# Performance work log

Hardware: AMD Instinct MI355X
Metric: run time of the kernel (lower is better)

## Reference

```python
import jax, jax.numpy as jnp
import numpy as np

B, S, D, H = 4, 1024, 1024, 16
DK = D // H
MASK_WEIGHT_0 = 1.0   # weight for key-type 0 (from (weight, mask_mat) tuple)
MASK_WEIGHT_1 = 0.5   # weight for key-type 1
NEG_INF = -1.0e9


def setup_inputs() -> dict:
    key = jax.random.key(0)
    ks = jax.random.split(key, 10)
    wscale = 0.02
    return {
        "query": jax.random.normal(ks[0], (B, S, D), jnp.float32),
        "key_x": jax.random.normal(ks[1], (B, S, D), jnp.float32),
        "value": jax.random.normal(ks[2], (B, S, D), jnp.float32),
        "mask0": jax.random.randint(ks[3], (B, S, S), 0, 2, jnp.int32),
        "mask1": jax.random.randint(ks[4], (B, S, S), 0, 2, jnp.int32),
        "Wq":  wscale * jax.random.normal(ks[5], (D, D), jnp.float32),
        "Wk0": wscale * jax.random.normal(ks[6], (D, D), jnp.float32),
        "Wk1": wscale * jax.random.normal(ks[7], (D, D), jnp.float32),
        "Wv":  wscale * jax.random.normal(ks[8], (D, D), jnp.float32),
        "Wo":  wscale * jax.random.normal(ks[9], (D, D), jnp.float32),
    }


def _heads(x, W):
    # torch nn.Linear: x @ W.T ; then view(B,S,H,DK).transpose(1,2)
    return (x @ W.T).reshape(B, S, H, DK).transpose(0, 2, 1, 3)  # [B,H,S,DK]


def reference(query, key_x, value, mask0, mask1, Wq, Wk0, Wk1, Wv, Wo):
    q = _heads(query, Wq)          # [B,H,S,DK]
    k0 = _heads(key_x, Wk0)
    k1 = _heads(key_x, Wk1)
    v = _heads(value, Wv)
    scale = 1.0 / jnp.sqrt(jnp.float32(DK))

    def masked_score(k, mask, weight):
        s = jnp.einsum('bhqd,bhkd->bhqk', q, k) * scale       # [B,H,S,S]
        keep = (mask != 0)[:, None, :, :]                     # broadcast over heads
        # (score * weight*keep).masked_fill(mask==0, -1e9)
        return jnp.where(keep, s * weight, NEG_INF)

    scores = masked_score(k0, mask0, MASK_WEIGHT_0) + masked_score(k1, mask1, MASK_WEIGHT_1)
    p_attn = jax.nn.sigmoid(scores)                           # activation='sigmoid'
    x = jnp.einsum('bhqk,bhkd->bhqd', p_attn, v)              # [B,H,S,DK]
    x = x.transpose(0, 2, 1, 3).reshape(B, S, D)
    return x @ Wo.T                                            # output_linear (dropout p=0)
```

## Files before the change

### kernel.cpp

```cpp
#include <hip/hip_runtime.h>

#define B_  4
#define S_  1024
#define D_  1024
#define H_  16
#define DK_ 64

typedef __attribute__((ext_vector_type(8)))  short bf16x8;
typedef __attribute__((ext_vector_type(4)))  short bf16x4;
typedef __attribute__((ext_vector_type(4)))  float f32x4;
typedef __attribute__((ext_vector_type(16))) float f32x16;

static __device__ __forceinline__ unsigned short f2bf(float f) {
  union { float f; unsigned u; } v; v.f = f;
  unsigned r = v.u + 0x7FFFu + ((v.u >> 16) & 1u);
  return (unsigned short)(r >> 16);
}

static __device__ __forceinline__ unsigned cvtpk(float lo, float hi) {
  unsigned r;
  asm("v_cvt_pk_bf16_f32 %0, %1, %2" : "=v"(r) : "v"(lo), "v"(hi));
  return r;
}
static __device__ __forceinline__ void plswap(unsigned &a, unsigned &b) {
  asm volatile("v_permlane32_swap_b32 %0, %1" : "+v"(a), "+v"(b));
}

typedef __attribute__((address_space(1))) const void gc_t;
typedef __attribute__((address_space(3))) void lds_t;
static __device__ __forceinline__ void gload_lds16(const void* g, void* l) {
  __builtin_amdgcn_global_load_lds((gc_t*)g, (lds_t*)l, 16, 0, 0);
}

#define TM_ (1u << 22)
#define WM_ (1u << 20)

#define CEXP_ (-0.18033688011112042f)

__global__ __launch_bounds__(256)
void prep(const float* __restrict__ q, const float* __restrict__ k,
          const float* __restrict__ v,
          const float* __restrict__ w0, const float* __restrict__ w1,
          const float* __restrict__ w2, const float* __restrict__ w3,
          const float* __restrict__ w4, unsigned short* __restrict__ out,
          const int* __restrict__ m0, const int* __restrict__ m1,
          unsigned long long* __restrict__ pk)
{
  if (blockIdx.x < 8192) {
    const size_t u = ((size_t)blockIdx.x * 256 + threadIdx.x) * 8;
    unsigned short t[8];
    unsigned short* dst;
    size_t off;
    if (u < (size_t)3 * TM_) {
      int seg = (int)(u >> 22); off = u & (TM_ - 1);
      const float* src = seg == 0 ? q : (seg == 1 ? k : v);
      dst = out + (size_t)seg * TM_ + off;
      float4 f0 = *(const float4*)(src + off);
      float4 f1 = *(const float4*)(src + off + 4);
      t[0]=f2bf(f0.x); t[1]=f2bf(f0.y); t[2]=f2bf(f0.z); t[3]=f2bf(f0.w);
      t[4]=f2bf(f1.x); t[5]=f2bf(f1.y); t[6]=f2bf(f1.z); t[7]=f2bf(f1.w);
    } else {
      size_t uu = u - (size_t)3 * TM_;
      int seg = (int)(uu >> 20); off = uu & (WM_ - 1);
      dst = out + (size_t)3 * TM_ + (size_t)seg * WM_ + off;
      if (seg == 1) {
        float4 a0 = *(const float4*)(w1 + off);
        float4 a1 = *(const float4*)(w1 + off + 4);
        float4 b0 = *(const float4*)(w2 + off);
        float4 b1 = *(const float4*)(w2 + off + 4);
        t[0]=f2bf(a0.x+0.5f*b0.x); t[1]=f2bf(a0.y+0.5f*b0.y);
        t[2]=f2bf(a0.z+0.5f*b0.z); t[3]=f2bf(a0.w+0.5f*b0.w);
        t[4]=f2bf(a1.x+0.5f*b1.x); t[5]=f2bf(a1.y+0.5f*b1.y);
        t[6]=f2bf(a1.z+0.5f*b1.z); t[7]=f2bf(a1.w+0.5f*b1.w);
      } else {
        const float* src = seg == 0 ? w0 : (seg == 2 ? w3 : w4);
        float4 f0 = *(const float4*)(src + off);
        float4 f1 = *(const float4*)(src + off + 4);
        t[0]=f2bf(f0.x); t[1]=f2bf(f0.y); t[2]=f2bf(f0.z); t[3]=f2bf(f0.w);
        t[4]=f2bf(f1.x); t[5]=f2bf(f1.y); t[6]=f2bf(f1.z); t[7]=f2bf(f1.w);
      }
    }
    *(bf16x8*)dst = *(bf16x8*)t;
  } else {
    const int bidm = blockIdx.x - 8192;
    const int wid  = bidm * 4 + (threadIdx.x >> 6);
    const int lane = threadIdx.x & 63;
    const int word = wid & 15, row = wid >> 4;
    const size_t g = (size_t)row * S_ + word * 64 + lane;
    const bool bit = (m0[g] != 0) & (m1[g] != 0);
    const unsigned long long m = __ballot(bit);
    if (lane == 0) pk[wid] = m;
  }
}

__global__ __launch_bounds__(256, 4)
void proj_gemm(const unsigned short* __restrict__ qbf,
               const unsigned short* __restrict__ kbf,
               const unsigned short* __restrict__ vbf,
               const unsigned short* __restrict__ wbf,
               unsigned short* __restrict__ Qb, unsigned short* __restrict__ Kh,
               unsigned short* __restrict__ Vth)
{
  __shared__ unsigned short As[128][64];
  __shared__ unsigned short Ws[128][64];

  const int tid = threadIdx.x, bid = blockIdx.x;
  const int xcd = bid & 7, c = bid >> 3;
  const int L = xcd * 96 + c;
  const int which = L >> 8;
  const int rem = L & 255;
  const int nt = rem >> 5, mt = rem & 31;
  const int m0 = mt * 128, n0 = nt * 128;
  const int w = tid >> 6, l = tid & 63;
  const int lr = l & 15, lg = l >> 4;
  const int wr = w >> 1, wc = w & 1;

  const unsigned short* A = (which == 0) ? qbf : (which == 1) ? kbf : vbf;
  const unsigned short* W = wbf + (size_t)which * WM_;

  const f32x4 fzero = {0.f, 0.f, 0.f, 0.f};
  f32x4 acc[4][4];
#pragma unroll
  for (int m = 0; m < 4; m++)
#pragma unroll
    for (int n = 0; n < 4; n++) acc[m][n] = fzero;

  const int srow8 = l >> 3;
  const int sg    = ((l & 7) ^ srow8) * 8;
  const int rc0 = ((lg)     ^ (lr & 7)) * 8;
  const int rc1 = ((4 + lg) ^ (lr & 7)) * 8;

  const unsigned short* aBase = A + (size_t)(m0 + w*32 + srow8) * 1024 + sg;
  const unsigned short* wBase = W + (size_t)(n0 + w*32 + srow8) * 1024 + sg;

  for (int kk = 0; kk < 1024; kk += 64) {
#pragma unroll
    for (int cc = 0; cc < 4; ++cc)
      gload_lds16(aBase + (size_t)cc * 8 * 1024 + kk, &As[w*32 + cc*8][0]);
#pragma unroll
    for (int cc = 0; cc < 4; ++cc)
      gload_lds16(wBase + (size_t)cc * 8 * 1024 + kk, &Ws[w*32 + cc*8][0]);
    __syncthreads();

#pragma unroll
    for (int ks = 0; ks < 2; ++ks) {
      const int rc = ks ? rc1 : rc0;
      bf16x8 af[4], bfr[4];
#pragma unroll
      for (int m = 0; m < 4; m++) af[m]  = *(const bf16x8*)&As[wr*64 + m*16 + lr][rc];
#pragma unroll
      for (int n = 0; n < 4; n++) bfr[n] = *(const bf16x8*)&Ws[wc*64 + n*16 + lr][rc];
#pragma unroll
      for (int m = 0; m < 4; m++)
#pragma unroll
        for (int n = 0; n < 4; n++)
          acc[m][n] = __builtin_amdgcn_mfma_f32_16x16x32_bf16(af[m], bfr[n], acc[m][n], 0, 0, 0);
    }
    __syncthreads();
  }

  if (which == 2) {
#pragma unroll
    for (int m = 0; m < 4; m++) {
      const int row = m0 + wr*64 + m*16 + lg*4;
      const int b = row >> 10, s = row & 1023;
#pragma unroll
      for (int n = 0; n < 4; n++) {
        const int col = n0 + wc*64 + n*16 + lr;
        const int h = col >> 6, dk = col & 63;
        unsigned short tv[4] = {f2bf(acc[m][n][0]), f2bf(acc[m][n][1]),
                                f2bf(acc[m][n][2]), f2bf(acc[m][n][3])};
        const size_t a = ((size_t)((b*H_ + h)*DK_ + dk)) * S_
                       + (size_t)(s & ~63) + ((((s >> 3) & 7) ^ (dk & 7)) << 3) + (s & 7);
        *(bf16x4*)(Vth + a) = *(bf16x4*)tv;
      }
    }
  } else if (which == 0) {
#pragma unroll
    for (int m = 0; m < 4; m++) {
      const int row = m0 + wr*64 + m*16 + lg*4;
#pragma unroll
      for (int n = 0; n < 4; n++) {
        const int col = n0 + wc*64 + n*16 + lr;
#pragma unroll
        for (int r = 0; r < 4; r++)
          Qb[(size_t)(row + r) * 1024 + col] = f2bf(acc[m][n][r]);
      }
    }
  } else {
#pragma unroll
    for (int m = 0; m < 4; m++) {
      const int row = m0 + wr*64 + m*16 + lg*4;
#pragma unroll
      for (int n = 0; n < 4; n++) {
        const int col = n0 + wc*64 + n*16 + lr;
        const int h = col >> 6, dk = col & 63;
#pragma unroll
        for (int r = 0; r < 4; r++) {
          const int rr = row + r;
          const int b = rr >> 10, s = rr & 1023;
          const size_t a = ((size_t)((b*H_ + h)*S_ + s)) * 64
                         + (((dk >> 3) ^ (s & 7)) << 3) + (dk & 7);
          Kh[a] = f2bf(acc[m][n][r]);
        }
      }
    }
  }
}

__global__ __launch_bounds__(256, 4)
void out_gemm(const unsigned short* __restrict__ A,
              const unsigned short* __restrict__ W, float* __restrict__ C)
{
  __shared__ unsigned short As[128][64];
  __shared__ unsigned short Ws2[64][64];

  const int tid = threadIdx.x, bid = blockIdx.x;
  const int xcd = bid & 7, idx = bid >> 3;
  const int mt = (xcd << 2) | (idx & 3);
  const int nt = idx >> 2;
  const int m0 = mt * 128, n0 = nt * 64;
  const int w = tid >> 6, l = tid & 63;
  const int lr = l & 15, lg = l >> 4;
  const int wr = w >> 1, wc = w & 1;

  const f32x4 fzero = {0.f, 0.f, 0.f, 0.f};
  f32x4 acc[4][2];
#pragma unroll
  for (int m = 0; m < 4; m++)
#pragma unroll
    for (int n = 0; n < 2; n++) acc[m][n] = fzero;

  const int srow8 = l >> 3;
  const int sg    = ((l & 7) ^ srow8) * 8;
  const int rc0 = ((lg)     ^ (lr & 7)) * 8;
  const int rc1 = ((4 + lg) ^ (lr & 7)) * 8;

  const unsigned short* aBase = A + (size_t)(m0 + w*32 + srow8) * 1024 + sg;
  const unsigned short* wBase = W + (size_t)(n0 + w*16 + srow8) * 1024 + sg;

  for (int kk = 0; kk < 1024; kk += 64) {
#pragma unroll
    for (int cc = 0; cc < 4; ++cc)
      gload_lds16(aBase + (size_t)cc * 8 * 1024 + kk, &As[w*32 + cc*8][0]);
#pragma unroll
    for (int cc = 0; cc < 2; ++cc)
      gload_lds16(wBase + (size_t)cc * 8 * 1024 + kk, &Ws2[w*16 + cc*8][0]);
    __syncthreads();

#pragma unroll
    for (int ks = 0; ks < 2; ++ks) {
      const int rc = ks ? rc1 : rc0;
      bf16x8 af[4], bfr[2];
#pragma unroll
      for (int m = 0; m < 4; m++) af[m]  = *(const bf16x8*)&As[wr*64 + m*16 + lr][rc];
#pragma unroll
      for (int n = 0; n < 2; n++) bfr[n] = *(const bf16x8*)&Ws2[wc*32 + n*16 + lr][rc];
#pragma unroll
      for (int m = 0; m < 4; m++)
#pragma unroll
        for (int n = 0; n < 2; n++)
          acc[m][n] = __builtin_amdgcn_mfma_f32_16x16x32_bf16(af[m], bfr[n], acc[m][n], 0, 0, 0);
    }
    __syncthreads();
  }

#pragma unroll
  for (int m = 0; m < 4; m++) {
    const int row = m0 + wr*64 + m*16 + lg*4;
#pragma unroll
    for (int n = 0; n < 2; n++) {
      const int col = n0 + wc*32 + n*16 + lr;
#pragma unroll
      for (int r = 0; r < 4; r++)
        C[(size_t)(row + r) * 1024 + col] = acc[m][n][r];
    }
  }
}

__global__ __launch_bounds__(256)
void attn_kernel(const unsigned short* __restrict__ Q,
                 const unsigned short* __restrict__ Kh,
                 const unsigned short* __restrict__ Vth,
                 const unsigned long long* __restrict__ mpk,
                 unsigned short* __restrict__ X)
{
  __shared__ unsigned short Ks[2][4096];
  __shared__ unsigned short Vs[2][4096];

  const int tid  = threadIdx.x;
  const int bid0 = blockIdx.x;
  const int bid = ((bid0 & 7) << 6) | (bid0 >> 3);
  const int qt = bid & 7, h = (bid >> 3) & 15, b = bid >> 7;
  const int q0 = qt * 128;
  const int w = tid >> 6, lw = tid & 63;
  const int l31 = lw & 31, hh = lw >> 5, l7 = lw & 7;
  const int bh = b * H_ + h;

  bf16x8 qf[4];
  {
    const unsigned short* qp = Q + ((size_t)(b*S_ + q0 + w*32 + l31)) * D_ + h*DK_ + hh*8;
#pragma unroll
    for (int ds = 0; ds < 4; ++ds) qf[ds] = *(const bf16x8*)(qp + ds*16);
  }
  const size_t mbase = ((size_t)(b*S_ + q0 + w*32 + l31)) * 16;

  f32x16 acc0, acc1;
#pragma unroll
  for (int r = 0; r < 16; ++r) { acc0[r] = 0.f; acc1[r] = 0.f; }

  const unsigned short* gp[4];
  unsigned short* lb[4];
  int stp[4];
#pragma unroll
  for (int c = 0; c < 4; ++c) {
    const int e = w*4 + c;
    const int bu = e >> 3, s = e & 7;
    lb[c] = (bu == 0 ? &Ks[0][0] : &Vs[0][0]) + s*512;
    if (bu == 0) {
      gp[c]  = Kh + ((size_t)bh * S_) * 64 + s*512 + lw*8;
      stp[c] = 4096;
    } else {
      gp[c]  = Vth + ((size_t)(bh*DK_ + s*8 + (lw >> 3))) * S_ + (lw & 7) * 8;
      stp[c] = 64;
    }
  }

#define STAGE(nxt)                                                     \
  {                                                                    \
    _Pragma("unroll")                                                  \
    for (int c = 0; c < 4; ++c) {                                      \
      gload_lds16(gp[c], lb[c] + (nxt)*4096);                          \
      gp[c] += stp[c];                                                 \
    }                                                                  \
  }

  STAGE(0);
  __syncthreads();
  unsigned long long mw = mpk[mbase];
  int cur = 0;

  for (int t = 0; t < 16; ++t) {
    unsigned long long mw_n = 0;
    if (t < 15) { STAGE(cur ^ 1); mw_n = mpk[mbase + t + 1]; }

#pragma unroll
    for (int sub = 0; sub < 2; ++sub) {
      const int rbase = (sub*32 + l31) * 64;
      f32x16 sv;
#pragma unroll
      for (int r = 0; r < 16; ++r) sv[r] = 0.f;
      __builtin_amdgcn_s_setprio(1);
#pragma unroll
      for (int ds = 0; ds < 4; ++ds) {
        const int g = (((ds*2 + hh) ^ l7)) * 8;
        const bf16x8 kf = *(const bf16x8*)&Ks[cur][rbase + g];
        sv = __builtin_amdgcn_mfma_f32_32x32x16_bf16(kf, qf[ds], sv, 0, 0, 0);
      }
      __builtin_amdgcn_s_setprio(0);

      const unsigned am = (unsigned)(mw >> (sub*32 + 4*hh));
      float p[16];
#pragma unroll
      for (int r = 0; r < 16; ++r) {
        const int cbit = (r & 3) + 8*(r >> 2);
        const float e  = __builtin_amdgcn_exp2f(CEXP_ * sv[r]);
        const float pr = __builtin_amdgcn_rcpf(1.0f + e);
        p[r] = ((am >> cbit) & 1u) ? pr : 0.f;
      }

      bf16x8 pa[2];
#pragma unroll
      for (int ks = 0; ks < 2; ++ks) {
        const int a0 = ks*8;
        unsigned u0 = cvtpk(p[a0+0], p[a0+1]);
        unsigned u1 = cvtpk(p[a0+2], p[a0+3]);
        unsigned u2 = cvtpk(p[a0+4], p[a0+5]);
        unsigned u3 = cvtpk(p[a0+6], p[a0+7]);
        plswap(u0, u2);
        plswap(u1, u3);
        union { unsigned u[4]; bf16x8 v; } pu;
        pu.u[0] = u0; pu.u[1] = u1; pu.u[2] = u2; pu.u[3] = u3;
        pa[ks] = pu.v;
      }

      __builtin_amdgcn_s_setprio(1);
#pragma unroll
      for (int ks = 0; ks < 2; ++ks) {
        const int g = ((sub*4 + ks*2 + hh) ^ l7) * 8;
        const bf16x8 vb0 = *(const bf16x8*)&Vs[cur][(l31)      * 64 + g];
        const bf16x8 vb1 = *(const bf16x8*)&Vs[cur][(32 + l31) * 64 + g];
        acc0 = __builtin_amdgcn_mfma_f32_32x32x16_bf16(pa[ks], vb0, acc0, 0, 0, 0);
        acc1 = __builtin_amdgcn_mfma_f32_32x32x16_bf16(pa[ks], vb1, acc1, 0, 0, 0);
      }
      __builtin_amdgcn_s_setprio(0);
    }

    if (t < 15) {
      __syncthreads();
      mw = mw_n;
      cur ^= 1;
    }
  }
#undef STAGE

#pragma unroll
  for (int r = 0; r < 16; ++r) {
    const int qrow = q0 + w*32 + (r & 3) + 8*(r >> 2) + 4*hh;
    unsigned short* xp = X + ((size_t)(b*S_ + qrow)) * D_ + h*DK_ + l31;
    xp[0]  = f2bf(acc0[r]);
    xp[32] = f2bf(acc1[r]);
  }
}

extern "C" void kernel_launch(void* const* d_in, const int* in_sizes, int n_in,
                              void* d_out, int out_size, void* d_ws, size_t ws_size,
                              hipStream_t stream)
{
  const float* query = (const float*)d_in[0];
  const float* key_x = (const float*)d_in[1];
  const float* value = (const float*)d_in[2];
  const int*   mask0 = (const int*)d_in[3];
  const int*   mask1 = (const int*)d_in[4];
  const float* Wq    = (const float*)d_in[5];
  const float* Wk0   = (const float*)d_in[6];
  const float* Wk1   = (const float*)d_in[7];
  const float* Wv    = (const float*)d_in[8];
  const float* Wo    = (const float*)d_in[9];

  unsigned short* ws = (unsigned short*)d_ws;
  unsigned short* qbf = ws;
  unsigned short* kbf = ws + (size_t)TM_;
  unsigned short* vbf = ws + (size_t)2 * TM_;
  unsigned short* wbf = ws + (size_t)3 * TM_;
  unsigned short* Qb  = ws + (size_t)3 * TM_ + 4 * WM_;
  unsigned short* Kh  = Qb  + (size_t)TM_;
  unsigned short* Vth = Kh  + (size_t)TM_;
  unsigned long long* mpk = (unsigned long long*)(Vth + (size_t)TM_);
  unsigned short* Xb = qbf;

  prep<<<dim3(8192 + 16384), dim3(256), 0, stream>>>(
      query, key_x, value, Wq, Wk0, Wk1, Wv, Wo, ws, mask0, mask1, mpk);

  proj_gemm<<<dim3(768), dim3(256), 0, stream>>>(qbf, kbf, vbf, wbf,
                                                 Qb, Kh, Vth);

  attn_kernel<<<dim3(B_ * H_ * (S_ / 128)), dim3(256), 0, stream>>>(
      Qb, Kh, Vth, mpk, Xb);

  out_gemm<<<dim3(512), dim3(256), 0, stream>>>(Xb, wbf + (size_t)3 * WM_,
                                                (float*)d_out);
}
```

Before: 111.2 us.

## Split attention key range across two warp groups and fold score scale into Wq

The attention kernel now runs 512 threads per block, with two groups of four waves each processing half of the key sequence. Each group has its own double-buffered K/V shared-memory tiles, and the partial outputs are combined through shared memory before writing. Separately, the exp2 scaling constant is folded into the bf16 conversion of Wq, which removes one multiply per score element. The split doubles wave-level parallelism per block to hide latency, at the cost of more shared memory, an extra reduction, and lower bf16 precision from the pre-scaled weights.

```diff
diff --git a/kernel.cpp b/kernel.cpp
--- a/kernel.cpp
+++ b/kernel.cpp
@@ -63,7 +63,14 @@
       size_t uu = u - (size_t)3 * TM_;
       int seg = (int)(uu >> 20); off = uu & (WM_ - 1);
       dst = out + (size_t)3 * TM_ + (size_t)seg * WM_ + off;
-      if (seg == 1) {
+      if (seg == 0) {
+        float4 f0 = *(const float4*)(w0 + off);
+        float4 f1 = *(const float4*)(w0 + off + 4);
+        t[0]=f2bf(CEXP_*f0.x); t[1]=f2bf(CEXP_*f0.y);
+        t[2]=f2bf(CEXP_*f0.z); t[3]=f2bf(CEXP_*f0.w);
+        t[4]=f2bf(CEXP_*f1.x); t[5]=f2bf(CEXP_*f1.y);
+        t[6]=f2bf(CEXP_*f1.z); t[7]=f2bf(CEXP_*f1.w);
+      } else if (seg == 1) {
         float4 a0 = *(const float4*)(w1 + off);
         float4 a1 = *(const float4*)(w1 + off + 4);
         float4 b0 = *(const float4*)(w2 + off);
@@ -73,7 +80,7 @@
         t[4]=f2bf(a1.x+0.5f*b1.x); t[5]=f2bf(a1.y+0.5f*b1.y);
         t[6]=f2bf(a1.z+0.5f*b1.z); t[7]=f2bf(a1.w+0.5f*b1.w);
       } else {
-        const float* src = seg == 0 ? w0 : (seg == 2 ? w3 : w4);
+        const float* src = (seg == 2) ? w3 : w4;
         float4 f0 = *(const float4*)(src + off);
         float4 f1 = *(const float4*)(src + off + 4);
         t[0]=f2bf(f0.x); t[1]=f2bf(f0.y); t[2]=f2bf(f0.z); t[3]=f2bf(f0.w);
@@ -278,32 +285,33 @@
   }
 }
 
-__global__ __launch_bounds__(256)
+__global__ __launch_bounds__(512)
 void attn_kernel(const unsigned short* __restrict__ Q,
                  const unsigned short* __restrict__ Kh,
                  const unsigned short* __restrict__ Vth,
                  const unsigned long long* __restrict__ mpk,
                  unsigned short* __restrict__ X)
 {
-  __shared__ unsigned short Ks[2][4096];
-  __shared__ unsigned short Vs[2][4096];
+  __shared__ unsigned short Ks[2][2][4096];
+  __shared__ unsigned short Vs[2][2][4096];
 
   const int tid  = threadIdx.x;
   const int bid0 = blockIdx.x;
   const int bid = ((bid0 & 7) << 6) | (bid0 >> 3);
   const int qt = bid & 7, h = (bid >> 3) & 15, b = bid >> 7;
   const int q0 = qt * 128;
-  const int w = tid >> 6, lw = tid & 63;
+  const int w8 = tid >> 6, lw = tid & 63;
+  const int grp = w8 >> 2, qw = w8 & 3;
   const int l31 = lw & 31, hh = lw >> 5, l7 = lw & 7;
   const int bh = b * H_ + h;
 
   bf16x8 qf[4];
   {
-    const unsigned short* qp = Q + ((size_t)(b*S_ + q0 + w*32 + l31)) * D_ + h*DK_ + hh*8;
+    const unsigned short* qp = Q + ((size_t)(b*S_ + q0 + qw*32 + l31)) * D_ + h*DK_ + hh*8;
 #pragma unroll
     for (int ds = 0; ds < 4; ++ds) qf[ds] = *(const bf16x8*)(qp + ds*16);
   }
-  const size_t mbase = ((size_t)(b*S_ + q0 + w*32 + l31)) * 16;
+  const size_t mbase = ((size_t)(b*S_ + q0 + qw*32 + l31)) * 16 + grp*8;
 
   f32x16 acc0, acc1;
 #pragma unroll
@@ -314,14 +322,14 @@
   int stp[4];
 #pragma unroll
   for (int c = 0; c < 4; ++c) {
-    const int e = w*4 + c;
+    const int e = qw*4 + c;
     const int bu = e >> 3, s = e & 7;
-    lb[c] = (bu == 0 ? &Ks[0][0] : &Vs[0][0]) + s*512;
+    lb[c] = (bu == 0 ? &Ks[grp][0][0] : &Vs[grp][0][0]) + s*512;
     if (bu == 0) {
-      gp[c]  = Kh + ((size_t)bh * S_) * 64 + s*512 + lw*8;
+      gp[c]  = Kh + (size_t)bh * 65536 + grp*32768 + s*512 + lw*8;
       stp[c] = 4096;
     } else {
-      gp[c]  = Vth + ((size_t)(bh*DK_ + s*8 + (lw >> 3))) * S_ + (lw & 7) * 8;
+      gp[c]  = Vth + ((size_t)(bh*DK_ + s*8 + (lw >> 3))) * S_ + grp*512 + (lw & 7) * 8;
       stp[c] = 64;
     }
   }
@@ -340,9 +348,9 @@
   unsigned long long mw = mpk[mbase];
   int cur = 0;
 
-  for (int t = 0; t < 16; ++t) {
+  for (int t = 0; t < 8; ++t) {
     unsigned long long mw_n = 0;
-    if (t < 15) { STAGE(cur ^ 1); mw_n = mpk[mbase + t + 1]; }
+    if (t < 7) { STAGE(cur ^ 1); mw_n = mpk[mbase + t + 1]; }
 
 #pragma unroll
     for (int sub = 0; sub < 2; ++sub) {
@@ -354,7 +362,7 @@
 #pragma unroll
       for (int ds = 0; ds < 4; ++ds) {
         const int g = (((ds*2 + hh) ^ l7)) * 8;
-        const bf16x8 kf = *(const bf16x8*)&Ks[cur][rbase + g];
+        const bf16x8 kf = *(const bf16x8*)&Ks[grp][cur][rbase + g];
         sv = __builtin_amdgcn_mfma_f32_32x32x16_bf16(kf, qf[ds], sv, 0, 0, 0);
       }
       __builtin_amdgcn_s_setprio(0);
@@ -364,7 +372,7 @@
 #pragma unroll
       for (int r = 0; r < 16; ++r) {
         const int cbit = (r & 3) + 8*(r >> 2);
-        const float e  = __builtin_amdgcn_exp2f(CEXP_ * sv[r]);
+        const float e  = __builtin_amdgcn_exp2f(sv[r]);
         const float pr = __builtin_amdgcn_rcpf(1.0f + e);
         p[r] = ((am >> cbit) & 1u) ? pr : 0.f;
       }
@@ -388,15 +396,15 @@
 #pragma unroll
       for (int ks = 0; ks < 2; ++ks) {
         const int g = ((sub*4 + ks*2 + hh) ^ l7) * 8;
-        const bf16x8 vb0 = *(const bf16x8*)&Vs[cur][(l31)      * 64 + g];
-        const bf16x8 vb1 = *(const bf16x8*)&Vs[cur][(32 + l31) * 64 + g];
+        const bf16x8 vb0 = *(const bf16x8*)&Vs[grp][cur][(l31)      * 64 + g];
+        const bf16x8 vb1 = *(const bf16x8*)&Vs[grp][cur][(32 + l31) * 64 + g];
         acc0 = __builtin_amdgcn_mfma_f32_32x32x16_bf16(pa[ks], vb0, acc0, 0, 0, 0);
         acc1 = __builtin_amdgcn_mfma_f32_32x32x16_bf16(pa[ks], vb1, acc1, 0, 0, 0);
       }
       __builtin_amdgcn_s_setprio(0);
     }
 
-    if (t < 15) {
+    if (t < 7) {
       __syncthreads();
       mw = mw_n;
       cur ^= 1;
@@ -404,12 +412,35 @@
   }
 #undef STAGE
 
-#pragma unroll
-  for (int r = 0; r < 16; ++r) {
-    const int qrow = q0 + w*32 + (r & 3) + 8*(r >> 2) + 4*hh;
-    unsigned short* xp = X + ((size_t)(b*S_ + qrow)) * D_ + h*DK_ + l31;
-    xp[0]  = f2bf(acc0[r]);
-    xp[32] = f2bf(acc1[r]);
+  __syncthreads();
+  float2* cmb = (float2*)&Ks[0][0][0];
+  if (grp == 1) {
+#pragma unroll
+    for (int i = 0; i < 8; ++i)
+      cmb[(qw*16 + i)*64 + lw] = make_float2(acc0[2*i], acc0[2*i+1]);
+#pragma unroll
+    for (int i = 0; i < 8; ++i)
+      cmb[(qw*16 + 8 + i)*64 + lw] = make_float2(acc1[2*i], acc1[2*i+1]);
+  }
+  __syncthreads();
+  if (grp == 0) {
+#pragma unroll
+    for (int i = 0; i < 8; ++i) {
+      float2 v = cmb[(qw*16 + i)*64 + lw];
+      acc0[2*i] += v.x; acc0[2*i+1] += v.y;
+    }
+#pragma unroll
+    for (int i = 0; i < 8; ++i) {
+      float2 v = cmb[(qw*16 + 8 + i)*64 + lw];
+      acc1[2*i] += v.x; acc1[2*i+1] += v.y;
+    }
+#pragma unroll
+    for (int r = 0; r < 16; ++r) {
+      const int qrow = q0 + qw*32 + (r & 3) + 8*(r >> 2) + 4*hh;
+      unsigned short* xp = X + ((size_t)(b*S_ + qrow)) * D_ + h*DK_ + l31;
+      xp[0]  = f2bf(acc0[r]);
+      xp[32] = f2bf(acc1[r]);
+    }
   }
 }
 
@@ -445,7 +476,7 @@
   proj_gemm<<<dim3(768), dim3(256), 0, stream>>>(qbf, kbf, vbf, wbf,
                                                  Qb, Kh, Vth);
 
-  attn_kernel<<<dim3(B_ * H_ * (S_ / 128)), dim3(256), 0, stream>>>(
+  attn_kernel<<<dim3(B_ * H_ * (S_ / 128)), dim3(512), 0, stream>>>(
       Qb, Kh, Vth, mpk, Xb);
 
   out_gemm<<<dim3(512), dim3(256), 0, stream>>>(Xb, wbf + (size_t)3 * WM_,
```

After: 103.1 us. -7.3%, faster.
